# Kernel optimization log

Hardware: AMD Instinct MI355X
Metric: run time of the kernel (lower is better)

The kernel has to match this reference:

```python
import jax, jax.numpy as jnp
import numpy as np

NUM_EMBEDDINGS = 2048
EMBEDDING_DIM = 256
COMMITMENT_COST = 0.25


def setup_inputs() -> dict:
    key = jax.random.key(0)
    k1, k2 = jax.random.split(key)
    z_e = jax.random.normal(k1, (64, EMBEDDING_DIM, 32, 32), dtype=jnp.float32)
    # nn.Embedding weight initialized uniform(-1/K, 1/K)
    bound = 1.0 / NUM_EMBEDDINGS
    codebook = jax.random.uniform(k2, (NUM_EMBEDDINGS, EMBEDDING_DIM),
                                  dtype=jnp.float32, minval=-bound, maxval=bound)
    return {"z_e": z_e, "codebook": codebook}


def reference(z_e, codebook):
    B, C, H, W = z_e.shape  # C == embedding_dim
    K = codebook.shape[0]
    sg = jax.lax.stop_gradient

    # [B, C, H, W] -> [B*H*W, C]
    z_e_flat = jnp.transpose(z_e, (0, 2, 3, 1)).reshape(-1, C)

    # squared L2 distances: ||z||^2 - 2 z E^T + ||E||^2  -> [N, K]
    distances = (jnp.sum(z_e_flat ** 2, axis=1, keepdims=True)
                 - 2.0 * jnp.matmul(z_e_flat, codebook.T)
                 + jnp.sum(codebook ** 2, axis=1))
    indices = jnp.argmin(distances, axis=1)  # [N]

    encodings = jax.nn.one_hot(indices, K, dtype=z_e_flat.dtype)  # [N, K]
    z_q_flat = codebook[indices]  # [N, C] embedding gather
    z_q = jnp.transpose(z_q_flat.reshape(B, H, W, C), (0, 3, 1, 2))

    codebook_loss = jnp.mean((z_q_flat - sg(z_e_flat)) ** 2)
    commitment_loss = jnp.mean((sg(z_q_flat) - z_e_flat) ** 2)
    loss = codebook_loss + COMMITMENT_COST * commitment_loss

    e_mean = jnp.mean(encodings, axis=0)  # [K]
    perplexity = jnp.exp(-jnp.sum(e_mean * jnp.log(e_mean + 1e-10)))

    # straight-through estimator
    z_q_st = z_e + sg(z_q - z_e)
    return z_q_st, loss, perplexity, encodings
```

## Files before the change

### kernel.cpp

```cpp
#include <hip/hip_runtime.h>
#include <hip/hip_bf16.h>
#include <math.h>

#define NTOT 65536
#define KCB  2048
#define CDIM 256
#define HW   1024

#define OUT_LOSS 16777216
#define OUT_PERP 16777217
#define OUT_ENC  16777218

#define ZB_OFF_F  16777232
#define CBB_OFF_F 33554448

#define WS_SROW 0
#define WS_CK   262144
#define WS_IDX  270336
#define WS_CNT  532480
#define WS_PART 540672

#define MARGIN 3e-3f
#define CAP 2048

typedef __attribute__((ext_vector_type(8))) short short8;
typedef __attribute__((ext_vector_type(4))) float f32x4;

__device__ inline unsigned enc_f(float x) {
    unsigned u = __float_as_uint(x);
    return (u & 0x80000000u) ? ~u : (u | 0x80000000u);
}
__device__ inline float dec_f(unsigned e) {
    unsigned u = (e & 0x80000000u) ? (e ^ 0x80000000u) : ~e;
    return __uint_as_float(u);
}

__device__ inline void lds_min_u64(unsigned long long* p, unsigned long long v) {
    unsigned long long old = *p;
    while (v < old) {
        unsigned long long assumed = old;
        old = atomicCAS(p, assumed, v);
        if (old == assumed) break;
    }
}

__global__ __launch_bounds__(256) void k_prep(const float* __restrict__ z, const float* __restrict__ cb,
                                              ushort* __restrict__ zb, ushort* __restrict__ cbb,
                                              float* __restrict__ ck, float* __restrict__ srow,
                                              int* __restrict__ cntK) {
    __shared__ float tile[64][65];
    const int tid = threadIdx.x;
    const int bid = blockIdx.x;
    if (bid < 512) {
        int wv = tid >> 6, lane = tid & 63;
        int r = bid * 4 + wv;
        const float* row = cb + (size_t)r * CDIM;
        float4 v = *(const float4*)(row + lane * 4);
        ushort4 o;
        __hip_bfloat16 h;
        h = __float2bfloat16(v.x); o.x = *(ushort*)&h;
        h = __float2bfloat16(v.y); o.y = *(ushort*)&h;
        h = __float2bfloat16(v.z); o.z = *(ushort*)&h;
        h = __float2bfloat16(v.w); o.w = *(ushort*)&h;
        *(ushort4*)(cbb + (size_t)r * CDIM + lane * 4) = o;
        float s = v.x*v.x + v.y*v.y + v.z*v.z + v.w*v.w;
        for (int off = 32; off >= 1; off >>= 1) s += __shfl_down(s, off, 64);
        if (lane == 0) ck[r] = s;
        if (lane == 1) cntK[r] = 0;
    } else if (bid < 768) {
        int n = (bid - 512) * 256 + tid;
        int b = n >> 10, hw = n & 1023;
        const float* base = z + (size_t)b * (CDIM * HW) + hw;
        float s = 0.f;
#pragma unroll 8
        for (int c = 0; c < CDIM; ++c) { float v = base[(size_t)c * HW]; s = fmaf(v, v, s); }
        srow[n] = s;
    } else {
        int zbid = bid - 768;
        int hwT = zbid & 15, cT = (zbid >> 4) & 3, b = zbid >> 6;
        int c0 = cT * 64, hw0 = hwT * 64;
        int w = tid >> 6, hw = tid & 63;
#pragma unroll
        for (int l = 0; l < 16; ++l) {
            int c = l * 4 + w;
            tile[c][hw] = z[((size_t)b * CDIM + (c0 + c)) * HW + hw0 + hw];
        }
        __syncthreads();
        int r = tid >> 2, g = tid & 3;
        union { ushort u[16]; int4 v[2]; } pk;
#pragma unroll
        for (int j = 0; j < 16; ++j) {
            __hip_bfloat16 h = __float2bfloat16(tile[g * 16 + j][r]);
            pk.u[j] = *(ushort*)&h;
        }
        size_t n = (size_t)b * HW + hw0 + r;
        ushort* dst = zb + n * CDIM + c0 + g * 16;
        *(int4*)(dst) = pk.v[0];
        *(int4*)(dst + 8) = pk.v[1];
    }
}

__global__ __launch_bounds__(256, 2) void k_mfma_argmin(
    const ushort* __restrict__ zb, const ushort* __restrict__ cbb,
    const float* __restrict__ z, const float* __restrict__ cb,
    const float* __restrict__ srow, const float* __restrict__ ckg,
    int* __restrict__ indices, int* __restrict__ cntK)
{
    __shared__ unsigned long long wmin[4][64];
    __shared__ float thrRow[64];
    __shared__ int   candRK[CAP];
    __shared__ int   cnt;
    __shared__ int   allscan;
    __shared__ unsigned long long best[64];

    const int tid = threadIdx.x;
    const int w = tid >> 6, lane = tid & 63;
    const int col = lane & 15, quad = lane >> 4;
    const int n0 = blockIdx.x * 64;

    short8 areg[4][8];
#pragma unroll
    for (int nt = 0; nt < 4; ++nt)
#pragma unroll
        for (int cs = 0; cs < 8; ++cs)
            areg[nt][cs] = *(const short8*)(zb + ((size_t)(n0 + nt * 16 + col)) * CDIM + cs * 32 + quad * 8);

    float m1[16], m2[16]; int k1[16];
#pragma unroll
    for (int s = 0; s < 16; ++s) { m1[s] = INFINITY; m2[s] = INFINITY; k1[s] = 0; }

    for (int k0 = 0; k0 < KCB; k0 += 128) {
        const int kb = k0 + w * 32;
#pragma unroll
        for (int kt = 0; kt < 2; ++kt) {
            const int kk = kb + kt * 16 + col;
            const ushort* bbase = cbb + (size_t)kk * CDIM + quad * 8;
            short8 bfrag[8];
#pragma unroll
            for (int cs = 0; cs < 8; ++cs) bfrag[cs] = *(const short8*)(bbase + cs * 32);
            f32x4 acc[4];
#pragma unroll
            for (int nt = 0; nt < 4; ++nt) acc[nt] = (f32x4){0.f, 0.f, 0.f, 0.f};
#pragma unroll
            for (int cs = 0; cs < 8; ++cs)
#pragma unroll
                for (int nt = 0; nt < 4; ++nt)
                    acc[nt] = __builtin_amdgcn_mfma_f32_16x16x32_bf16(areg[nt][cs], bfrag[cs], acc[nt], 0, 0, 0);
            const float ckv = ckg[kk];
#pragma unroll
            for (int nt = 0; nt < 4; ++nt)
#pragma unroll
                for (int r = 0; r < 4; ++r) {
                    float dt = fmaf(-2.0f, acc[nt][r], ckv);
                    const int s = nt * 4 + r;
                    bool c = dt < m1[s];
                    m2[s] = fminf(m2[s], fmaxf(dt, m1[s]));
                    m1[s] = fminf(m1[s], dt);
                    k1[s] = c ? kk : k1[s];
                }
        }
    }

#pragma unroll
    for (int s = 0; s < 16; ++s) {
        unsigned long long v = ((unsigned long long)enc_f(m1[s]) << 32) | (unsigned)k1[s];
#pragma unroll
        for (int m = 1; m <= 8; m <<= 1) {
            unsigned long long o = __shfl_xor(v, m, 64);
            v = (o < v) ? o : v;
        }
        if (col == 0) wmin[w][(s >> 2) * 16 + quad * 4 + (s & 3)] = v;
    }
    if (tid == 0) { cnt = 0; allscan = 0; }
    if (tid < 64) best[tid] = ~0ull;
    __syncthreads();
    if (tid < 64) {
        unsigned long long v = wmin[0][tid];
        unsigned long long o = wmin[1][tid]; v = (o < v) ? o : v;
        o = wmin[2][tid]; v = (o < v) ? o : v;
        o = wmin[3][tid]; v = (o < v) ? o : v;
        thrRow[tid] = dec_f((unsigned)(v >> 32)) + MARGIN;
    }
    __syncthreads();

#pragma unroll
    for (int s = 0; s < 16; ++s) {
        const int row = (s >> 2) * 16 + quad * 4 + (s & 3);
        const float thr = thrRow[row];
        if (m1[s] <= thr) {
            int p = atomicAdd(&cnt, 1);
            if (p < CAP) candRK[p] = (row << 16) | k1[s];
        }
        if (m2[s] <= thr) {
            const int kt = s & 1;
            (void)kt;
            int p = atomicAdd(&cnt, 32);
            if (p + 32 <= CAP) {
#pragma unroll
                for (int k0i = 0; k0i < 16; ++k0i) {
                    int kbase = k0i * 128 + w * 32 + col;
                    candRK[p + 2 * k0i]     = (row << 16) | kbase;
                    candRK[p + 2 * k0i + 1] = (row << 16) | (kbase + 16);
                }
            }
        }
    }
    __syncthreads();
    if (cnt > CAP) { if (tid == 0) allscan = 1; }
    __syncthreads();
    const int nc = allscan ? 0 : min(cnt, CAP);

    const int b = n0 >> 10, hw0 = n0 & 1023;
    for (int t = tid; t < nc; t += 256) {
        const int rc = candRK[t];
        const int row = rc >> 16, k = rc & 0xFFFF;
        const float* zp = z + (size_t)b * (CDIM * HW) + hw0 + row;
        const float* cp = cb + (size_t)k * CDIM;
        float m = 0.f;
#pragma unroll 8
        for (int c = 0; c < CDIM; ++c) m = fmaf(zp[(size_t)c << 10], cp[c], m);
        float d = (srow[n0 + row] - 2.0f * m) + ckg[k];
        unsigned long long pk = ((unsigned long long)__float_as_uint(d) << 32) | (unsigned)k;
        lds_min_u64(&best[row], pk);
    }
    if (allscan) {
        for (int row = 0; row < 64; ++row) {
            const float sr = srow[n0 + row];
            const float* zp = z + (size_t)b * (CDIM * HW) + hw0 + row;
            for (int kq = 0; kq < 8; ++kq) {
                int k = kq * 256 + tid;
                const float* cp = cb + (size_t)k * CDIM;
                float m = 0.f;
#pragma unroll 8
                for (int c = 0; c < CDIM; ++c) m = fmaf(zp[(size_t)c << 10], cp[c], m);
                float d = (sr - 2.0f * m) + ckg[k];
                unsigned long long pk = ((unsigned long long)__float_as_uint(d) << 32) | (unsigned)k;
                lds_min_u64(&best[row], pk);
            }
        }
    }
    __syncthreads();
    if (tid < 64) {
        int bk = (int)(best[tid] & 0xFFFFFFFFull);
        indices[n0 + tid] = bk;
        atomicAdd(&cntK[bk], 1);
    }
}

__global__ __launch_bounds__(256, 2) void k_gather(const float* __restrict__ z, const float* __restrict__ cb,
                                                   const int* __restrict__ idx, float* __restrict__ out0,
                                                   double* __restrict__ part) {
    __shared__ float qt[CDIM * 64];
    __shared__ double sh[256];
    const int tid = threadIdx.x;
    const int nl = tid & 63, cg = tid >> 6;
    const int n0 = blockIdx.x * 64;
    const int b = n0 >> 10, hw0 = n0 & 1023;
    const int k = idx[n0 + nl];
    const float* crow = cb + (size_t)k * CDIM + cg * 64;
#pragma unroll
    for (int j4 = 0; j4 < 16; ++j4) {
        float4 v = *(const float4*)(crow + j4 * 4);
        int c = cg * 64 + j4 * 4;
        qt[(c + 0) * 64 + nl] = v.x;
        qt[(c + 1) * 64 + nl] = v.y;
        qt[(c + 2) * 64 + nl] = v.z;
        qt[(c + 3) * 64 + nl] = v.w;
    }
    __syncthreads();
    double acc = 0.0;
    const size_t ebase = ((size_t)b * CDIM) * HW + hw0 + nl;
#pragma unroll 4
    for (int j = 0; j < 64; ++j) {
        int c = cg * 64 + j;
        size_t e = ebase + ((size_t)c << 10);
        float ze = z[e];
        float q = qt[c * 64 + nl];
        float d = q - ze;
        out0[e] = ze + d;
        acc += (double)d * (double)d;
    }
    sh[tid] = acc;
    __syncthreads();
    for (int s = 128; s > 0; s >>= 1) {
        if (tid < s) sh[tid] += sh[tid + s];
        __syncthreads();
    }
    if (tid == 0) part[blockIdx.x] = sh[0];
}

__global__ __launch_bounds__(256) void k_encodings(const int* __restrict__ idx, float4* __restrict__ p4,
                                                   float* __restrict__ tail) {
    __shared__ int sidx[17];
    const int tid = threadIdx.x;
    const size_t g0 = (size_t)blockIdx.x * 8192;
    const long f0 = 4L * (long)g0 - 2;
    int nlo = (int)(f0 >> 11); if (nlo < 0) nlo = 0;
    if (tid < 17) { int n = nlo + tid; sidx[tid] = (n < NTOT) ? idx[n] : -1; }
    __syncthreads();
    const float4 zv = make_float4(0.f, 0.f, 0.f, 0.f);
    for (int i = 0; i < 32; ++i) {
        size_t g = g0 + (size_t)i * 256 + tid;
        long fe = 4L * (long)g - 2;
        float4 v = zv;
        if (fe < 0) {
            int kk = sidx[0];
            if (kk == 0) v.z = 1.f;
            if (kk == 1) v.w = 1.f;
        } else {
            int n = (int)(fe >> 11);
            int k0c = (int)(fe & 2047);
            if (k0c >= 2045) {
#pragma unroll
                for (int j = 0; j < 4; ++j) {
                    long fej = fe + j;
                    int nj = (int)(fej >> 11);
                    int kj = (int)(fej & 2047);
                    int li = nj - nlo;
                    int kk = (li >= 0 && li < 17) ? sidx[li] : -2;
                    ((float*)&v)[j] = (kk == kj) ? 1.f : 0.f;
                }
            } else {
                int d = sidx[n - nlo] - k0c;
                if (d >= 0 && d < 4) ((float*)&v)[d] = 1.f;
            }
        }
        p4[g] = v;
    }
    if (blockIdx.x == 0 && tid == 0) {
        int kk = idx[NTOT - 1];
        tail[0] = (kk == 2046) ? 1.f : 0.f;
        tail[1] = (kk == 2047) ? 1.f : 0.f;
    }
}

__global__ __launch_bounds__(256) void k_finalize(const double* __restrict__ part, const int* __restrict__ cnt,
                                                  float* __restrict__ out) {
    __shared__ double sh[256];
    double a = 0.0;
    for (int i = threadIdx.x; i < 1024; i += 256) a += part[i];
    sh[threadIdx.x] = a; __syncthreads();
    for (int s = 128; s > 0; s >>= 1) { if (threadIdx.x < s) sh[threadIdx.x] += sh[threadIdx.x + s]; __syncthreads(); }
    double total = sh[0];
    __syncthreads();
    double p = 0.0;
    for (int i = threadIdx.x; i < 2048; i += 256) {
        double pm = (double)cnt[i] / 65536.0;
        p += pm * log(pm + 1e-10);
    }
    sh[threadIdx.x] = p; __syncthreads();
    for (int s = 128; s > 0; s >>= 1) { if (threadIdx.x < s) sh[threadIdx.x] += sh[threadIdx.x + s]; __syncthreads(); }
    if (threadIdx.x == 0) {
        double mean = total / ((double)NTOT * (double)CDIM);
        out[OUT_LOSS] = (float)(mean * 1.25);
        out[OUT_PERP] = (float)exp(-sh[0]);
    }
}

extern "C" void kernel_launch(void* const* d_in, const int* in_sizes, int n_in,
                              void* d_out, int out_size, void* d_ws, size_t ws_size,
                              hipStream_t stream) {
    const float* z  = (const float*)d_in[0];
    const float* cb = (const float*)d_in[1];
    float* out = (float*)d_out;
    char* ws = (char*)d_ws;
    float*  srow = (float*)(ws + WS_SROW);
    float*  ck   = (float*)(ws + WS_CK);
    int*    idx  = (int*)(ws + WS_IDX);
    int*    cnt  = (int*)(ws + WS_CNT);
    double* part = (double*)(ws + WS_PART);
    ushort* zb  = (ushort*)(out + ZB_OFF_F);
    ushort* cbb = (ushort*)(out + CBB_OFF_F);

    hipLaunchKernelGGL(k_prep,        dim3(4864), dim3(256), 0, stream, z, cb, zb, cbb, ck, srow, cnt);
    hipLaunchKernelGGL(k_mfma_argmin, dim3(1024), dim3(256), 0, stream, zb, cbb, z, cb, srow, ck, idx, cnt);
    hipLaunchKernelGGL(k_gather,      dim3(1024), dim3(256), 0, stream, z, cb, idx, out, part);
    hipLaunchKernelGGL(k_encodings,   dim3(4096), dim3(256), 0, stream, idx, (float4*)(out + OUT_LOSS),
                       out + (OUT_LOSS + (size_t)33554432 * 4));
    hipLaunchKernelGGL(k_finalize,    dim3(1),    dim3(256), 0, stream, part, cnt, out);
}
```

Measured before the change: 929.9 us.

## Fuse z transpose, row norms, argmin and gather into one kernel via LDS tile

Each block now loads its 64-row z tile once into LDS, then builds bf16 MFMA operands, row norms, candidate rescoring and the straight-through output and loss from that tile. This removes the separate transposed-bf16 z buffer, the strided srow pass and the k_gather kernel, along with their global reads and writes of z. The cost is about 66KB of LDS per block for the z tile (CAP is halved to make room), which may cut occupancy below the 2-blocks-per-CU launch bound. The gather phase also adds an 8-step loop with barriers in which only one wave writes per step.

```diff
diff --git a/kernel.cpp b/kernel.cpp
--- a/kernel.cpp
+++ b/kernel.cpp
@@ -11,17 +11,15 @@
 #define OUT_PERP 16777217
 #define OUT_ENC  16777218
 
-#define ZB_OFF_F  16777232
 #define CBB_OFF_F 33554448
 
-#define WS_SROW 0
 #define WS_CK   262144
 #define WS_IDX  270336
 #define WS_CNT  532480
 #define WS_PART 540672
 
 #define MARGIN 3e-3f
-#define CAP 2048
+#define CAP 1024
 
 typedef __attribute__((ext_vector_type(8))) short short8;
 typedef __attribute__((ext_vector_type(4))) float f32x4;
@@ -44,86 +42,86 @@
     }
 }
 
-__global__ __launch_bounds__(256) void k_prep(const float* __restrict__ z, const float* __restrict__ cb,
-                                              ushort* __restrict__ zb, ushort* __restrict__ cbb,
-                                              float* __restrict__ ck, float* __restrict__ srow,
-                                              int* __restrict__ cntK) {
-    __shared__ float tile[64][65];
+__global__ __launch_bounds__(256) void k_prep_cb(const float* __restrict__ cb, ushort* __restrict__ cbb,
+                                                 float* __restrict__ ck, int* __restrict__ cntK) {
     const int tid = threadIdx.x;
-    const int bid = blockIdx.x;
-    if (bid < 512) {
-        int wv = tid >> 6, lane = tid & 63;
-        int r = bid * 4 + wv;
-        const float* row = cb + (size_t)r * CDIM;
-        float4 v = *(const float4*)(row + lane * 4);
-        ushort4 o;
-        __hip_bfloat16 h;
-        h = __float2bfloat16(v.x); o.x = *(ushort*)&h;
-        h = __float2bfloat16(v.y); o.y = *(ushort*)&h;
-        h = __float2bfloat16(v.z); o.z = *(ushort*)&h;
-        h = __float2bfloat16(v.w); o.w = *(ushort*)&h;
-        *(ushort4*)(cbb + (size_t)r * CDIM + lane * 4) = o;
-        float s = v.x*v.x + v.y*v.y + v.z*v.z + v.w*v.w;
-        for (int off = 32; off >= 1; off >>= 1) s += __shfl_down(s, off, 64);
-        if (lane == 0) ck[r] = s;
-        if (lane == 1) cntK[r] = 0;
-    } else if (bid < 768) {
-        int n = (bid - 512) * 256 + tid;
-        int b = n >> 10, hw = n & 1023;
-        const float* base = z + (size_t)b * (CDIM * HW) + hw;
-        float s = 0.f;
-#pragma unroll 8
-        for (int c = 0; c < CDIM; ++c) { float v = base[(size_t)c * HW]; s = fmaf(v, v, s); }
-        srow[n] = s;
-    } else {
-        int zbid = bid - 768;
-        int hwT = zbid & 15, cT = (zbid >> 4) & 3, b = zbid >> 6;
-        int c0 = cT * 64, hw0 = hwT * 64;
-        int w = tid >> 6, hw = tid & 63;
-#pragma unroll
-        for (int l = 0; l < 16; ++l) {
-            int c = l * 4 + w;
-            tile[c][hw] = z[((size_t)b * CDIM + (c0 + c)) * HW + hw0 + hw];
-        }
-        __syncthreads();
-        int r = tid >> 2, g = tid & 3;
-        union { ushort u[16]; int4 v[2]; } pk;
-#pragma unroll
-        for (int j = 0; j < 16; ++j) {
-            __hip_bfloat16 h = __float2bfloat16(tile[g * 16 + j][r]);
-            pk.u[j] = *(ushort*)&h;
-        }
-        size_t n = (size_t)b * HW + hw0 + r;
-        ushort* dst = zb + n * CDIM + c0 + g * 16;
-        *(int4*)(dst) = pk.v[0];
-        *(int4*)(dst + 8) = pk.v[1];
-    }
-}
-
-__global__ __launch_bounds__(256, 2) void k_mfma_argmin(
-    const ushort* __restrict__ zb, const ushort* __restrict__ cbb,
+    const int wv = tid >> 6, lane = tid & 63;
+    const int r = blockIdx.x * 4 + wv;
+    const float* row = cb + (size_t)r * CDIM;
+    float4 v = *(const float4*)(row + lane * 4);
+    ushort4 o;
+    __hip_bfloat16 h;
+    h = __float2bfloat16(v.x); o.x = *(ushort*)&h;
+    h = __float2bfloat16(v.y); o.y = *(ushort*)&h;
+    h = __float2bfloat16(v.z); o.z = *(ushort*)&h;
+    h = __float2bfloat16(v.w); o.w = *(ushort*)&h;
+    *(ushort4*)(cbb + (size_t)r * CDIM + lane * 4) = o;
+    float s = v.x*v.x + v.y*v.y + v.z*v.z + v.w*v.w;
+    for (int off = 32; off >= 1; off >>= 1) s += __shfl_down(s, off, 64);
+    if (lane == 0) ck[r] = s;
+    if (lane == 1) cntK[r] = 0;
+}
+
+__global__ __launch_bounds__(256, 2) void k_main(
     const float* __restrict__ z, const float* __restrict__ cb,
-    const float* __restrict__ srow, const float* __restrict__ ckg,
-    int* __restrict__ indices, int* __restrict__ cntK)
+    const ushort* __restrict__ cbb, const float* __restrict__ ckg,
+    int* __restrict__ indices, int* __restrict__ cntK,
+    float* __restrict__ out0, double* __restrict__ part)
 {
-    __shared__ unsigned long long wmin[4][64];
-    __shared__ float thrRow[64];
-    __shared__ int   candRK[CAP];
-    __shared__ int   cnt;
-    __shared__ int   allscan;
+    __shared__ float ztb[CDIM * 65];
+    __shared__ union {
+        struct {
+            unsigned long long wmin[4][64];
+            float thrRow[64];
+            float srowL[64];
+            int   candRK[CAP];
+        } p1;
+        float  qc[32 * 65];
+        double sh[256];
+    } u;
     __shared__ unsigned long long best[64];
+    __shared__ int cnt;
+    __shared__ int allscan;
 
     const int tid = threadIdx.x;
     const int w = tid >> 6, lane = tid & 63;
     const int col = lane & 15, quad = lane >> 4;
     const int n0 = blockIdx.x * 64;
+    const int b = n0 >> 10, hw0 = n0 & 1023;
+
+    {
+        const int hwq = tid & 15, csub = (tid >> 4) & 3;
+#pragma unroll
+        for (int i = 0; i < 16; ++i) {
+            const int c = w * 64 + i * 4 + csub;
+            float4 v = *(const float4*)(z + ((size_t)b * CDIM + c) * HW + hw0 + hwq * 4);
+            float* dst = ztb + c * 65 + hwq * 4;
+            dst[0] = v.x; dst[1] = v.y; dst[2] = v.z; dst[3] = v.w;
+        }
+    }
+    if (tid == 0) { cnt = 0; allscan = 0; }
+    __syncthreads();
 
     short8 areg[4][8];
 #pragma unroll
     for (int nt = 0; nt < 4; ++nt)
 #pragma unroll
-        for (int cs = 0; cs < 8; ++cs)
-            areg[nt][cs] = *(const short8*)(zb + ((size_t)(n0 + nt * 16 + col)) * CDIM + cs * 32 + quad * 8);
+        for (int cs = 0; cs < 8; ++cs) {
+            short8 a;
+#pragma unroll
+            for (int j = 0; j < 8; ++j) {
+                __hip_bfloat16 h = __float2bfloat16(ztb[(cs * 32 + quad * 8 + j) * 65 + nt * 16 + col]);
+                a[j] = *(ushort*)&h;
+            }
+            areg[nt][cs] = a;
+        }
+
+    if (tid < 64) {
+        float s = 0.f;
+#pragma unroll 8
+        for (int c = 0; c < CDIM; ++c) { float v = ztb[c * 65 + tid]; s = fmaf(v, v, s); }
+        u.p1.srowL[tid] = s;
+    }
 
     float m1[16], m2[16]; int k1[16];
 #pragma unroll
@@ -169,38 +167,35 @@
             unsigned long long o = __shfl_xor(v, m, 64);
             v = (o < v) ? o : v;
         }
-        if (col == 0) wmin[w][(s >> 2) * 16 + quad * 4 + (s & 3)] = v;
-    }
-    if (tid == 0) { cnt = 0; allscan = 0; }
+        if (col == 0) u.p1.wmin[w][(s >> 2) * 16 + quad * 4 + (s & 3)] = v;
+    }
     if (tid < 64) best[tid] = ~0ull;
     __syncthreads();
     if (tid < 64) {
-        unsigned long long v = wmin[0][tid];
-        unsigned long long o = wmin[1][tid]; v = (o < v) ? o : v;
-        o = wmin[2][tid]; v = (o < v) ? o : v;
-        o = wmin[3][tid]; v = (o < v) ? o : v;
-        thrRow[tid] = dec_f((unsigned)(v >> 32)) + MARGIN;
+        unsigned long long v = u.p1.wmin[0][tid];
+        unsigned long long o = u.p1.wmin[1][tid]; v = (o < v) ? o : v;
+        o = u.p1.wmin[2][tid]; v = (o < v) ? o : v;
+        o = u.p1.wmin[3][tid]; v = (o < v) ? o : v;
+        u.p1.thrRow[tid] = dec_f((unsigned)(v >> 32)) + MARGIN;
     }
     __syncthreads();
 
 #pragma unroll
     for (int s = 0; s < 16; ++s) {
         const int row = (s >> 2) * 16 + quad * 4 + (s & 3);
-        const float thr = thrRow[row];
+        const float thr = u.p1.thrRow[row];
         if (m1[s] <= thr) {
             int p = atomicAdd(&cnt, 1);
-            if (p < CAP) candRK[p] = (row << 16) | k1[s];
+            if (p < CAP) u.p1.candRK[p] = (row << 16) | k1[s];
         }
         if (m2[s] <= thr) {
-            const int kt = s & 1;
-            (void)kt;
             int p = atomicAdd(&cnt, 32);
             if (p + 32 <= CAP) {
 #pragma unroll
                 for (int k0i = 0; k0i < 16; ++k0i) {
                     int kbase = k0i * 128 + w * 32 + col;
-                    candRK[p + 2 * k0i]     = (row << 16) | kbase;
-                    candRK[p + 2 * k0i + 1] = (row << 16) | (kbase + 16);
+                    u.p1.candRK[p + 2 * k0i]     = (row << 16) | kbase;
+                    u.p1.candRK[p + 2 * k0i + 1] = (row << 16) | (kbase + 16);
                 }
             }
         }
@@ -210,29 +205,26 @@
     __syncthreads();
     const int nc = allscan ? 0 : min(cnt, CAP);
 
-    const int b = n0 >> 10, hw0 = n0 & 1023;
     for (int t = tid; t < nc; t += 256) {
-        const int rc = candRK[t];
+        const int rc = u.p1.candRK[t];
         const int row = rc >> 16, k = rc & 0xFFFF;
-        const float* zp = z + (size_t)b * (CDIM * HW) + hw0 + row;
         const float* cp = cb + (size_t)k * CDIM;
         float m = 0.f;
 #pragma unroll 8
-        for (int c = 0; c < CDIM; ++c) m = fmaf(zp[(size_t)c << 10], cp[c], m);
-        float d = (srow[n0 + row] - 2.0f * m) + ckg[k];
+        for (int c = 0; c < CDIM; ++c) m = fmaf(ztb[c * 65 + row], cp[c], m);
+        float d = (u.p1.srowL[row] - 2.0f * m) + ckg[k];
         unsigned long long pk = ((unsigned long long)__float_as_uint(d) << 32) | (unsigned)k;
         lds_min_u64(&best[row], pk);
     }
     if (allscan) {
         for (int row = 0; row < 64; ++row) {
-            const float sr = srow[n0 + row];
-            const float* zp = z + (size_t)b * (CDIM * HW) + hw0 + row;
+            const float sr = u.p1.srowL[row];
             for (int kq = 0; kq < 8; ++kq) {
                 int k = kq * 256 + tid;
                 const float* cp = cb + (size_t)k * CDIM;
                 float m = 0.f;
 #pragma unroll 8
-                for (int c = 0; c < CDIM; ++c) m = fmaf(zp[(size_t)c << 10], cp[c], m);
+                for (int c = 0; c < CDIM; ++c) m = fmaf(ztb[c * 65 + row], cp[c], m);
                 float d = (sr - 2.0f * m) + ckg[k];
                 unsigned long long pk = ((unsigned long long)__float_as_uint(d) << 32) | (unsigned)k;
                 lds_min_u64(&best[row], pk);
@@ -245,48 +237,41 @@
         indices[n0 + tid] = bk;
         atomicAdd(&cntK[bk], 1);
     }
-}
-
-__global__ __launch_bounds__(256, 2) void k_gather(const float* __restrict__ z, const float* __restrict__ cb,
-                                                   const int* __restrict__ idx, float* __restrict__ out0,
-                                                   double* __restrict__ part) {
-    __shared__ float qt[CDIM * 64];
-    __shared__ double sh[256];
-    const int tid = threadIdx.x;
-    const int nl = tid & 63, cg = tid >> 6;
-    const int n0 = blockIdx.x * 64;
-    const int b = n0 >> 10, hw0 = n0 & 1023;
-    const int k = idx[n0 + nl];
-    const float* crow = cb + (size_t)k * CDIM + cg * 64;
-#pragma unroll
-    for (int j4 = 0; j4 < 16; ++j4) {
-        float4 v = *(const float4*)(crow + j4 * 4);
-        int c = cg * 64 + j4 * 4;
-        qt[(c + 0) * 64 + nl] = v.x;
-        qt[(c + 1) * 64 + nl] = v.y;
-        qt[(c + 2) * 64 + nl] = v.z;
-        qt[(c + 3) * 64 + nl] = v.w;
-    }
-    __syncthreads();
+
+    const size_t ebase = ((size_t)b * CDIM) * HW + hw0 + lane;
+    const int krow = (int)(best[lane] & 0xFFFFFFFFull);
+    const float* crow = cb + (size_t)krow * CDIM;
     double acc = 0.0;
-    const size_t ebase = ((size_t)b * CDIM) * HW + hw0 + nl;
+    for (int q = 0; q < 8; ++q) {
+        {
+            float4 v0 = *(const float4*)(crow + q * 32 + w * 8);
+            float4 v1 = *(const float4*)(crow + q * 32 + w * 8 + 4);
+            float* dst = u.qc + (w * 8) * 65 + lane;
+            dst[0 * 65] = v0.x; dst[1 * 65] = v0.y; dst[2 * 65] = v0.z; dst[3 * 65] = v0.w;
+            dst[4 * 65] = v1.x; dst[5 * 65] = v1.y; dst[6 * 65] = v1.z; dst[7 * 65] = v1.w;
+        }
+        __syncthreads();
+        if (w == (q >> 1)) {
+            const int j0 = (q & 1) * 32;
 #pragma unroll 4
-    for (int j = 0; j < 64; ++j) {
-        int c = cg * 64 + j;
-        size_t e = ebase + ((size_t)c << 10);
-        float ze = z[e];
-        float q = qt[c * 64 + nl];
-        float d = q - ze;
-        out0[e] = ze + d;
-        acc += (double)d * (double)d;
-    }
-    sh[tid] = acc;
-    __syncthreads();
-    for (int s = 128; s > 0; s >>= 1) {
-        if (tid < s) sh[tid] += sh[tid + s];
+            for (int jj = 0; jj < 32; ++jj) {
+                const int c = w * 64 + j0 + jj;
+                float ze = ztb[c * 65 + lane];
+                float qv = u.qc[jj * 65 + lane];
+                float d = qv - ze;
+                out0[ebase + ((size_t)c << 10)] = ze + d;
+                acc += (double)d * (double)d;
+            }
+        }
         __syncthreads();
     }
-    if (tid == 0) part[blockIdx.x] = sh[0];
+    u.sh[tid] = acc;
+    __syncthreads();
+    for (int s2 = 128; s2 > 0; s2 >>= 1) {
+        if (tid < s2) u.sh[tid] += u.sh[tid + s2];
+        __syncthreads();
+    }
+    if (tid == 0) part[blockIdx.x] = u.sh[0];
 }
 
 __global__ __launch_bounds__(256) void k_encodings(const int* __restrict__ idx, float4* __restrict__ p4,
@@ -364,18 +349,15 @@
     const float* cb = (const float*)d_in[1];
     float* out = (float*)d_out;
     char* ws = (char*)d_ws;
-    float*  srow = (float*)(ws + WS_SROW);
     float*  ck   = (float*)(ws + WS_CK);
     int*    idx  = (int*)(ws + WS_IDX);
     int*    cnt  = (int*)(ws + WS_CNT);
     double* part = (double*)(ws + WS_PART);
-    ushort* zb  = (ushort*)(out + ZB_OFF_F);
     ushort* cbb = (ushort*)(out + CBB_OFF_F);
 
-    hipLaunchKernelGGL(k_prep,        dim3(4864), dim3(256), 0, stream, z, cb, zb, cbb, ck, srow, cnt);
-    hipLaunchKernelGGL(k_mfma_argmin, dim3(1024), dim3(256), 0, stream, zb, cbb, z, cb, srow, ck, idx, cnt);
-    hipLaunchKernelGGL(k_gather,      dim3(1024), dim3(256), 0, stream, z, cb, idx, out, part);
-    hipLaunchKernelGGL(k_encodings,   dim3(4096), dim3(256), 0, stream, idx, (float4*)(out + OUT_LOSS),
+    hipLaunchKernelGGL(k_prep_cb,   dim3(512),  dim3(256), 0, stream, cb, cbb, ck, cnt);
+    hipLaunchKernelGGL(k_main,      dim3(1024), dim3(256), 0, stream, z, cb, cbb, ck, idx, cnt, out, part);
+    hipLaunchKernelGGL(k_encodings, dim3(4096), dim3(256), 0, stream, idx, (float4*)(out + OUT_LOSS),
                        out + (OUT_LOSS + (size_t)33554432 * 4));
-    hipLaunchKernelGGL(k_finalize,    dim3(1),    dim3(256), 0, stream, part, cnt, out);
-}
+    hipLaunchKernelGGL(k_finalize,  dim3(1),    dim3(256), 0, stream, part, cnt, out);
+}
```

Result: faster. 862.7 us (-7.2%).
